# Optimization experiments

Hardware: AMD Instinct MI355X
Metric: run time of the kernel (lower is better)

## Reference

```python
import jax, jax.numpy as jnp
import numpy as np

D_MODEL = 1024
NUM_HEADS = 16
D_K = D_MODEL // NUM_HEADS


def setup_inputs() -> dict:
    key = jax.random.key(0)
    ks = jax.random.split(key, 5)
    B, S = 4, 2048
    scale = 1.0 / np.sqrt(D_MODEL)
    x = jax.random.normal(ks[0], (B, S, D_MODEL), dtype=jnp.float32)
    Wq = jax.random.normal(ks[1], (D_MODEL, D_MODEL), dtype=jnp.float32) * scale
    Wk = jax.random.normal(ks[2], (D_MODEL, D_MODEL), dtype=jnp.float32) * scale
    Wv = jax.random.normal(ks[3], (D_MODEL, D_MODEL), dtype=jnp.float32) * scale
    Wo = jax.random.normal(ks[4], (D_MODEL, D_MODEL), dtype=jnp.float32) * scale
    return {"x": x, "Wq": Wq, "Wk": Wk, "Wv": Wv, "Wo": Wo}


def reference(x, Wq, Wk, Wv, Wo):
    B, S, _ = x.shape
    # projections (torch Linear: y = x @ W^T, no bias)
    def proj(W):
        y = jnp.einsum('bsd,ed->bse', x, W)
        # split heads: (b, s, h*dk) -> (b, h, s, dk)
        return y.reshape(B, S, NUM_HEADS, D_K).transpose(0, 2, 1, 3)
    Q, K, V = proj(Wq), proj(Wk), proj(Wv)
    scores = jnp.einsum('bhqd,bhkd->bhqk', Q, K) / np.sqrt(D_K)
    causal = jnp.tril(jnp.ones((S, S), dtype=bool))
    scores = jnp.where(causal, scores, -jnp.inf)
    attn = jax.nn.softmax(scores, axis=-1)
    out = jnp.einsum('bhqk,bhkd->bhqd', attn, V)
    out = out.transpose(0, 2, 1, 3).reshape(B, S, D_MODEL)
    return jnp.einsum('bse,de->bsd', out, Wo)
```

## Files before the change

### kernel.cpp

```cpp
#include <hip/hip_runtime.h>
#include <hip/hip_bf16.h>

typedef __attribute__((ext_vector_type(8))) short short8;
typedef __attribute__((ext_vector_type(2))) float f32x2;
typedef __attribute__((ext_vector_type(4))) float f32x4;
typedef __attribute__((ext_vector_type(16))) float f32x16;

static constexpr int DM = 1024;
static constexpr int NH = 16;
static constexpr int DK = 64;
static constexpr int SL = 2048;
static constexpr int BB = 4;
static constexpr size_t QKV_ELEMS = (size_t)BB * NH * SL * DK;
static constexpr float NEG_BIG = -30000.0f;
static constexpr float SC_LOG2E = 0.125f * 1.44269504088896340736f;

union PackB { __hip_bfloat16 h[8]; uint4 u; };
union Pack4 { __hip_bfloat16 h[4]; uint2 u; };

typedef __attribute__((address_space(1))) unsigned int gu32;
typedef __attribute__((address_space(3))) unsigned int lu32;
__device__ __forceinline__ void async_copy16(const void* g, void* l) {
    __builtin_amdgcn_global_load_lds((gu32*)g, (lu32*)l, 16, 0, 0);
}

__device__ __forceinline__ unsigned cvt_pk_bf16(float lo, float hi) {
    unsigned r;
    asm("v_cvt_pk_bf16_f32 %0, %1, %2" : "=v"(r) : "v"(lo), "v"(hi));
    return r;
}
__device__ __forceinline__ void pl32_swap(unsigned &a, unsigned &b) {
    asm("v_permlane32_swap_b32 %0, %1" : "+v"(a), "+v"(b));
}

__global__ __launch_bounds__(256)
void cvt_all(const float* __restrict__ x,
             const float* __restrict__ wq, const float* __restrict__ wk,
             const float* __restrict__ wv, const float* __restrict__ wo,
             __hip_bfloat16* __restrict__ dst)
{
    const size_t i = (size_t)blockIdx.x * 256 + threadIdx.x;
    const float* src; size_t local;
    if (i < 2097152) { src = x; local = i; }
    else {
        const size_t j = i - 2097152;
        const int r = (int)(j >> 18);
        local = j & 262143;
        src = (r == 0) ? wq : (r == 1) ? wk : (r == 2) ? wv : wo;
    }
    float4 f = reinterpret_cast<const float4*>(src)[local];
    Pack4 p;
    p.h[0] = __float2bfloat16(f.x); p.h[1] = __float2bfloat16(f.y);
    p.h[2] = __float2bfloat16(f.z); p.h[3] = __float2bfloat16(f.w);
    reinterpret_cast<uint2*>(dst)[i] = p.u;
}

__global__ __launch_bounds__(256)
void gemm_qkv(const __hip_bfloat16* __restrict__ A,
              const __hip_bfloat16* __restrict__ W,
              __hip_bfloat16* __restrict__ q_out,
              __hip_bfloat16* __restrict__ k_out,
              __hip_bfloat16* __restrict__ v_out)
{
    __shared__ __hip_bfloat16 As[2][128 * 64];
    __shared__ __hip_bfloat16 Bs[2][128 * 64];
    const int tid  = threadIdx.x;
    const int m0   = blockIdx.x * 128;
    const int n0   = blockIdx.y * 128;
    const int w    = tid >> 6;
    const int lane = tid & 63;
    const int quad = lane >> 4;
    const int ln   = lane & 15;
    const int wm   = (w & 1) * 64;
    const int wn   = (w >> 1) * 64;
    const int srow = lane >> 3;
    const int sch  = ((lane & 7) ^ srow) * 8;

    f32x4 acc[4][4] = {};

    auto stage = [&](int buf, int k0) {
        #pragma unroll
        for (int j = 0; j < 4; j++) {
            const int rbase = w * 32 + j * 8;
            async_copy16(A + (size_t)(m0 + rbase + srow) * DM + k0 + sch,
                         &As[buf][rbase * 64]);
            async_copy16(W + (size_t)(n0 + rbase + srow) * DM + k0 + sch,
                         &Bs[buf][rbase * 64]);
        }
    };

    constexpr int NT = DM / 64;
    stage(0, 0);
    asm volatile("s_waitcnt vmcnt(0)" ::: "memory");
    __syncthreads();

    int cur = 0;
    for (int t = 0; t < NT; ++t) {
        if (t + 1 < NT) stage(cur ^ 1, (t + 1) * 64);

        #pragma unroll
        for (int ks = 0; ks < 2; ks++) {
            short8 a[4], b[4];
            #pragma unroll
            for (int i = 0; i < 4; i++)
                a[i] = *reinterpret_cast<const short8*>(
                    &As[cur][(wm + i*16 + ln) * 64 + (((ks*4 + quad) ^ (ln & 7)) * 8)]);
            #pragma unroll
            for (int j = 0; j < 4; j++)
                b[j] = *reinterpret_cast<const short8*>(
                    &Bs[cur][(wn + j*16 + ln) * 64 + (((ks*4 + quad) ^ (ln & 7)) * 8)]);
            __builtin_amdgcn_s_setprio(1);
            #pragma unroll
            for (int i = 0; i < 4; i++)
                #pragma unroll
                for (int j = 0; j < 4; j++)
                    acc[i][j] = __builtin_amdgcn_mfma_f32_16x16x32_bf16(a[i], b[j], acc[i][j], 0, 0, 0);
            __builtin_amdgcn_s_setprio(0);
        }

        if (t + 1 < NT) {
            asm volatile("s_waitcnt vmcnt(0)" ::: "memory");
            __syncthreads();
        }
        cur ^= 1;
    }

    #pragma unroll
    for (int i = 0; i < 4; i++) {
        #pragma unroll
        for (int j = 0; j < 4; j++) {
            #pragma unroll
            for (int r = 0; r < 4; r++) {
                const int m = m0 + wm + i*16 + quad*4 + r;
                const int n = n0 + wn + j*16 + ln;
                const int b_ = m >> 11;
                const int s  = m & 2047;
                const int which = n >> 10;
                const int nn = n & 1023;
                const int h  = nn >> 6;
                const int d  = nn & 63;
                if (which == 0) {
                    const __hip_bfloat16 v = __float2bfloat16(acc[i][j][r] * SC_LOG2E);
                    q_out[((size_t)((b_*NH + h)*SL + s))*DK + d] = v;
                } else if (which == 1) {
                    const __hip_bfloat16 v = __float2bfloat16(acc[i][j][r]);
                    k_out[((size_t)((b_*NH + h)*SL + s))*DK + d] = v;
                } else {
                    const __hip_bfloat16 v = __float2bfloat16(acc[i][j][r]);
                    v_out[((size_t)((b_*NH + h)*DK + d))*SL + s] = v;
                }
            }
        }
    }
}

__global__ __launch_bounds__(256)
void gemm_wo(const __hip_bfloat16* __restrict__ A,
             const __hip_bfloat16* __restrict__ W,
             float* __restrict__ outp)
{
    __shared__ __hip_bfloat16 As[2][128 * 64];
    __shared__ __hip_bfloat16 Bs[2][128 * 64];
    const int tid  = threadIdx.x;
    const int m0   = blockIdx.x * 128;
    const int n0   = blockIdx.y * 128;
    const int w    = tid >> 6;
    const int lane = tid & 63;
    const int quad = lane >> 4;
    const int ln   = lane & 15;
    const int wm   = (w & 1) * 64;
    const int wn   = (w >> 1) * 64;
    const int srow = lane >> 3;
    const int sch  = ((lane & 7) ^ srow) * 8;

    f32x4 acc[4][4] = {};

    auto stage = [&](int buf, int k0) {
        #pragma unroll
        for (int j = 0; j < 4; j++) {
            const int rbase = w * 32 + j * 8;
            async_copy16(A + (size_t)(m0 + rbase + srow) * DM + k0 + sch,
                         &As[buf][rbase * 64]);
            async_copy16(W + (size_t)(n0 + rbase + srow) * DM + k0 + sch,
                         &Bs[buf][rbase * 64]);
        }
    };

    constexpr int NT = DM / 64;
    stage(0, 0);
    asm volatile("s_waitcnt vmcnt(0)" ::: "memory");
    __syncthreads();

    int cur = 0;
    for (int t = 0; t < NT; ++t) {
        if (t + 1 < NT) stage(cur ^ 1, (t + 1) * 64);

        #pragma unroll
        for (int ks = 0; ks < 2; ks++) {
            short8 a[4], b[4];
            #pragma unroll
            for (int i = 0; i < 4; i++)
                a[i] = *reinterpret_cast<const short8*>(
                    &As[cur][(wm + i*16 + ln) * 64 + (((ks*4 + quad) ^ (ln & 7)) * 8)]);
            #pragma unroll
            for (int j = 0; j < 4; j++)
                b[j] = *reinterpret_cast<const short8*>(
                    &Bs[cur][(wn + j*16 + ln) * 64 + (((ks*4 + quad) ^ (ln & 7)) * 8)]);
            __builtin_amdgcn_s_setprio(1);
            #pragma unroll
            for (int i = 0; i < 4; i++)
                #pragma unroll
                for (int j = 0; j < 4; j++)
                    acc[i][j] = __builtin_amdgcn_mfma_f32_16x16x32_bf16(a[i], b[j], acc[i][j], 0, 0, 0);
            __builtin_amdgcn_s_setprio(0);
        }

        if (t + 1 < NT) {
            asm volatile("s_waitcnt vmcnt(0)" ::: "memory");
            __syncthreads();
        }
        cur ^= 1;
    }

    #pragma unroll
    for (int i = 0; i < 4; i++)
        #pragma unroll
        for (int j = 0; j < 4; j++)
            #pragma unroll
            for (int r = 0; r < 4; r++) {
                const int m = m0 + wm + i*16 + quad*4 + r;
                const int n = n0 + wn + j*16 + ln;
                outp[(size_t)m * DM + n] = acc[i][j][r];
            }
}

template<bool A_BF16, int MODE>
__global__ __launch_bounds__(256)
void gemm_bt(const void* __restrict__ Ap,
             const float* __restrict__ W,
             void* __restrict__ outp, float scl)
{
    __shared__ __hip_bfloat16 As[128][40];
    __shared__ __hip_bfloat16 Bs[128][40];
    const int tid  = threadIdx.x;
    const int m0   = blockIdx.x * 128;
    const int n0   = blockIdx.y * 128;
    const int w    = tid >> 6;
    const int lane = tid & 63;
    const int quad = lane >> 4;
    const int ln   = lane & 15;
    const int wm   = (w & 1) * 64;
    const int wn   = (w >> 1) * 64;
    const int lr   = tid >> 1;
    const int lc   = (tid & 1) * 16;

    f32x4 acc[4][4] = {};

    for (int k0 = 0; k0 < DM; k0 += 32) {
        if (A_BF16) {
            const uint4* ap = reinterpret_cast<const uint4*>(
                (const __hip_bfloat16*)Ap + (size_t)(m0 + lr) * DM + k0 + lc);
            uint4 a0 = ap[0], a1 = ap[1];
            *reinterpret_cast<uint4*>(&As[lr][lc])     = a0;
            *reinterpret_cast<uint4*>(&As[lr][lc + 8]) = a1;
        } else {
            const float4* ap = reinterpret_cast<const float4*>(
                (const float*)Ap + (size_t)(m0 + lr) * DM + k0 + lc);
            float4 f0 = ap[0], f1 = ap[1], f2 = ap[2], f3 = ap[3];
            PackB p0, p1;
            p0.h[0] = __float2bfloat16(f0.x); p0.h[1] = __float2bfloat16(f0.y);
            p0.h[2] = __float2bfloat16(f0.z); p0.h[3] = __float2bfloat16(f0.w);
            p0.h[4] = __float2bfloat16(f1.x); p0.h[5] = __float2bfloat16(f1.y);
            p0.h[6] = __float2bfloat16(f1.z); p0.h[7] = __float2bfloat16(f1.w);
            p1.h[0] = __float2bfloat16(f2.x); p1.h[1] = __float2bfloat16(f2.y);
            p1.h[2] = __float2bfloat16(f2.z); p1.h[3] = __float2bfloat16(f2.w);
            p1.h[4] = __float2bfloat16(f3.x); p1.h[5] = __float2bfloat16(f3.y);
            p1.h[6] = __float2bfloat16(f3.z); p1.h[7] = __float2bfloat16(f3.w);
            *reinterpret_cast<uint4*>(&As[lr][lc])     = p0.u;
            *reinterpret_cast<uint4*>(&As[lr][lc + 8]) = p1.u;
        }
        {
            const float4* wp = reinterpret_cast<const float4*>(
                W + (size_t)(n0 + lr) * DM + k0 + lc);
            float4 f0 = wp[0], f1 = wp[1], f2 = wp[2], f3 = wp[3];
            PackB p0, p1;
            p0.h[0] = __float2bfloat16(f0.x); p0.h[1] = __float2bfloat16(f0.y);
            p0.h[2] = __float2bfloat16(f0.z); p0.h[3] = __float2bfloat16(f0.w);
            p0.h[4] = __float2bfloat16(f1.x); p0.h[5] = __float2bfloat16(f1.y);
            p0.h[6] = __float2bfloat16(f1.z); p0.h[7] = __float2bfloat16(f1.w);
            p1.h[0] = __float2bfloat16(f2.x); p1.h[1] = __float2bfloat16(f2.y);
            p1.h[2] = __float2bfloat16(f2.z); p1.h[3] = __float2bfloat16(f2.w);
            p1.h[4] = __float2bfloat16(f3.x); p1.h[5] = __float2bfloat16(f3.y);
            p1.h[6] = __float2bfloat16(f3.z); p1.h[7] = __float2bfloat16(f3.w);
            *reinterpret_cast<uint4*>(&Bs[lr][lc])     = p0.u;
            *reinterpret_cast<uint4*>(&Bs[lr][lc + 8]) = p1.u;
        }
        __syncthreads();

        short8 a[4], b[4];
        #pragma unroll
        for (int i = 0; i < 4; i++)
            a[i] = *reinterpret_cast<const short8*>(&As[wm + i*16 + ln][quad*8]);
        #pragma unroll
        for (int j = 0; j < 4; j++)
            b[j] = *reinterpret_cast<const short8*>(&Bs[wn + j*16 + ln][quad*8]);
        #pragma unroll
        for (int i = 0; i < 4; i++)
            #pragma unroll
            for (int j = 0; j < 4; j++)
                acc[i][j] = __builtin_amdgcn_mfma_f32_16x16x32_bf16(a[i], b[j], acc[i][j], 0, 0, 0);
        __syncthreads();
    }

    #pragma unroll
    for (int i = 0; i < 4; i++) {
        #pragma unroll
        for (int j = 0; j < 4; j++) {
            #pragma unroll
            for (int r = 0; r < 4; r++) {
                const int m = m0 + wm + i*16 + quad*4 + r;
                const int n = n0 + wn + j*16 + ln;
                const float v = acc[i][j][r] * scl;
                if (MODE == 2) {
                    ((float*)outp)[(size_t)m * DM + n] = v;
                } else {
                    const int b_ = m >> 11;
                    const int s  = m & 2047;
                    const int h  = n >> 6;
                    const int d  = n & 63;
                    size_t idx;
                    if (MODE == 0) idx = ((size_t)((b_*NH + h)*SL + s))*DK + d;
                    else           idx = ((size_t)((b_*NH + h)*DK + d))*SL + s;
                    ((__hip_bfloat16*)outp)[idx] = __float2bfloat16(v);
                }
            }
        }
    }
}

__global__ __launch_bounds__(256)
void attn_causal(const __hip_bfloat16* __restrict__ Q,
                 const __hip_bfloat16* __restrict__ K,
                 const __hip_bfloat16* __restrict__ Vt,
                 __hip_bfloat16* __restrict__ O)
{
    __shared__ __hip_bfloat16 Ks[128 * 64];
    __shared__ __hip_bfloat16 Vs[64 * 128];

    const int tid  = threadIdx.x;
    const int w    = tid >> 6;
    const int lane = tid & 63;
    const int ln32 = lane & 31;
    const int hi   = lane >> 5;
    const int bh   = blockIdx.y;
    const int b_   = bh >> 4;
    const int h    = bh & 15;

    const __hip_bfloat16* Qb = Q  + (size_t)bh * SL * DK;
    const __hip_bfloat16* Kb = K  + (size_t)bh * SL * DK;
    const __hip_bfloat16* Vb = Vt + (size_t)bh * DK * SL;

    for (int pass = 0; pass < 2; ++pass) {
        const int qt    = (pass == 0) ? (int)blockIdx.x : 15 - (int)blockIdx.x;
        const int q0    = qt * 128;
        const int qbase = q0 + w * 32;
        const int qg    = qbase + ln32;

        short8 qf[4];
        #pragma unroll
        for (int dt = 0; dt < 4; dt++)
            qf[dt] = *reinterpret_cast<const short8*>(
                Qb + (size_t)qg * DK + dt*16 + hi*8);

        f32x16 o0 = {}, o1 = {};
        f32x2 ls2 = {0.f, 0.f};

        const int npair = qt + 1;

        for (int ip = 0; ip < npair; ++ip) {
            const int k0 = ip * 128;
            #pragma unroll
            for (int j = 0; j < 4; j++) {
                const int rb = w * 32 + j * 8;
                const int r  = rb + (lane >> 3);
                async_copy16(Kb + (size_t)(k0 + r) * DK + (((lane & 7) ^ (r & 7)) * 8),
                             &Ks[rb * 64]);
            }
            #pragma unroll
            for (int j = 0; j < 4; j++) {
                const int db = w * 16 + j * 4;
                const int d  = db + (lane >> 4);
                async_copy16(Vb + (size_t)d * SL + k0 + (((lane & 15) ^ (d & 7)) * 8),
                             &Vs[db * 128]);
            }
            asm volatile("s_waitcnt vmcnt(0)" ::: "memory");
            __syncthreads();

            #pragma unroll
            for (int hf = 0; hf < 2; hf++) {
                const int kh0 = k0 + hf * 64;
                if (kh0 > qbase + 31) continue;

                f32x16 s0 = {}, s1 = {};
                __builtin_amdgcn_s_setprio(1);
                #pragma unroll
                for (int dt = 0; dt < 4; dt++) {
                    const int r0 = hf*64 + ln32;
                    const int ch = (dt*2 + hi) ^ (ln32 & 7);
                    short8 kf0 = *reinterpret_cast<const short8*>(&Ks[r0*64 + ch*8]);
                    short8 kf1 = *reinterpret_cast<const short8*>(&Ks[(r0 + 32)*64 + ch*8]);
                    s0 = __builtin_amdgcn_mfma_f32_32x32x16_bf16(kf0, qf[dt], s0, 0, 0, 0);
                    s1 = __builtin_amdgcn_mfma_f32_32x32x16_bf16(kf1, qf[dt], s1, 0, 0, 0);
                }
                __builtin_amdgcn_s_setprio(0);

                const bool dodiag = (kh0 + 63 > qbase);
                if (dodiag) {
                    #pragma unroll
                    for (int r = 0; r < 16; r++) {
                        const int km = (r & 3) + 8*(r >> 2) + 4*hi;
                        float v0 = s0[r];
                        float v1 = s1[r];
                        if (kh0 + km      > qg) v0 = NEG_BIG;
                        if (kh0 + 32 + km > qg) v1 = NEG_BIG;
                        const float p0 = __builtin_amdgcn_exp2f(v0);
                        const float p1 = __builtin_amdgcn_exp2f(v1);
                        s0[r] = p0; s1[r] = p1;
                        ls2.x += p0; ls2.y += p1;
                    }
                } else {
                    #pragma unroll
                    for (int r = 0; r < 16; r++) {
                        const float p0 = __builtin_amdgcn_exp2f(s0[r]);
                        const float p1 = __builtin_amdgcn_exp2f(s1[r]);
                        s0[r] = p0; s1[r] = p1;
                        ls2.x += p0; ls2.y += p1;
                    }
                }

                __builtin_amdgcn_s_setprio(1);
                #pragma unroll
                for (int c = 0; c < 4; c++) {
                    const int R = 8 * (c & 1);
                    unsigned x0, x1, y0, y1;
                    if (c < 2) {
                        x0 = cvt_pk_bf16(s0[R+0], s0[R+1]);
                        x1 = cvt_pk_bf16(s0[R+2], s0[R+3]);
                        y0 = cvt_pk_bf16(s0[R+4], s0[R+5]);
                        y1 = cvt_pk_bf16(s0[R+6], s0[R+7]);
                    } else {
                        x0 = cvt_pk_bf16(s1[R+0], s1[R+1]);
                        x1 = cvt_pk_bf16(s1[R+2], s1[R+3]);
                        y0 = cvt_pk_bf16(s1[R+4], s1[R+5]);
                        y1 = cvt_pk_bf16(s1[R+6], s1[R+7]);
                    }
                    pl32_swap(x0, y0);
                    pl32_swap(x1, y1);
                    union { unsigned u[4]; short8 s8; } pf;
                    pf.u[0] = x0; pf.u[1] = x1; pf.u[2] = y0; pf.u[3] = y1;
                    const int vc = (hf*8 + c*2 + hi) ^ (ln32 & 7);
                    short8 vf0 = *reinterpret_cast<const short8*>(&Vs[ln32*128 + vc*8]);
                    short8 vf1 = *reinterpret_cast<const short8*>(&Vs[(32 + ln32)*128 + vc*8]);
                    o0 = __builtin_amdgcn_mfma_f32_32x32x16_bf16(vf0, pf.s8, o0, 0, 0, 0);
                    o1 = __builtin_amdgcn_mfma_f32_32x32x16_bf16(vf1, pf.s8, o1, 0, 0, 0);
                }
                __builtin_amdgcn_s_setprio(0);
            }
            __syncthreads();
        }

        float lsum = ls2.x + ls2.y;
        const float ls = lsum + __shfl_xor(lsum, 32, 64);
        const float rq = 1.0f / ls;

        __hip_bfloat16* Orow = O + (((size_t)b_ * SL + qg) * NH + h) * DK;
        #pragma unroll
        for (int g = 0; g < 4; g++) {
            uint2 pk0, pk1;
            pk0.x = cvt_pk_bf16(o0[4*g+0]*rq, o0[4*g+1]*rq);
            pk0.y = cvt_pk_bf16(o0[4*g+2]*rq, o0[4*g+3]*rq);
            pk1.x = cvt_pk_bf16(o1[4*g+0]*rq, o1[4*g+1]*rq);
            pk1.y = cvt_pk_bf16(o1[4*g+2]*rq, o1[4*g+3]*rq);
            *reinterpret_cast<uint2*>(Orow + 8*g + 4*hi)      = pk0;
            *reinterpret_cast<uint2*>(Orow + 32 + 8*g + 4*hi) = pk1;
        }
    }
}

extern "C" void kernel_launch(void* const* d_in, const int* in_sizes, int n_in,
                              void* d_out, int out_size, void* d_ws, size_t ws_size,
                              hipStream_t stream)
{
    const float* x  = (const float*)d_in[0];
    const float* Wq = (const float*)d_in[1];
    const float* Wk = (const float*)d_in[2];
    const float* Wv = (const float*)d_in[3];
    const float* Wo = (const float*)d_in[4];

    __hip_bfloat16* q_ws = (__hip_bfloat16*)d_ws;
    __hip_bfloat16* k_ws = q_ws + QKV_ELEMS;
    __hip_bfloat16* v_ws = k_ws + QKV_ELEMS;

    const dim3 gb(256);
    const size_t FAST_WS = (3 * QKV_ELEMS + QKV_ELEMS + 4 * (size_t)DM * DM)
                           * sizeof(__hip_bfloat16);

    if (ws_size >= FAST_WS) {
        __hip_bfloat16* xb  = v_ws + QKV_ELEMS;
        __hip_bfloat16* wqb = xb  + QKV_ELEMS;
        __hip_bfloat16* wob = wqb + 3 * (size_t)DM * DM;

        cvt_all<<<12288, 256, 0, stream>>>(x, Wq, Wk, Wv, Wo, xb);

        gemm_qkv<<<dim3(64, 24), gb, 0, stream>>>(xb, wqb, q_ws, k_ws, v_ws);

        attn_causal<<<dim3(8, BB*NH), 256, 0, stream>>>(q_ws, k_ws, v_ws, xb);

        gemm_wo<<<dim3(64, 8), gb, 0, stream>>>(xb, wob, (float*)d_out);
    } else {
        __hip_bfloat16* obuf = (__hip_bfloat16*)d_out;
        float*          fbuf = (float*)d_ws;
        const dim3 gg(64, 8);
        gemm_bt<false, 0><<<gg, gb, 0, stream>>>(x, Wq, q_ws, SC_LOG2E);
        gemm_bt<false, 0><<<gg, gb, 0, stream>>>(x, Wk, k_ws, 1.0f);
        gemm_bt<false, 1><<<gg, gb, 0, stream>>>(x, Wv, v_ws, 1.0f);
        attn_causal<<<dim3(8, BB*NH), 256, 0, stream>>>(q_ws, k_ws, v_ws, obuf);
        gemm_bt<true, 2><<<gg, gb, 0, stream>>>(obuf, Wo, fbuf, 1.0f);
        (void)hipMemcpyAsync(d_out, fbuf, QKV_ELEMS * sizeof(float),
                             hipMemcpyDeviceToDevice, stream);
    }
}
```

Baseline: 249.9 us.

## Use 256x128 GEMM tiles with 512 threads and a triple-buffered async pipeline

Both bf16 projection GEMMs (QKV and output) now use 512-thread blocks that compute 256x128 output tiles, with eight waves arranged 4x2. Shared memory becomes a three-stage ring, so loads run two K-tiles ahead. Each wait uses vmcnt(6) to wait only for the older stage, and sched_barriers surround the raw s_barrier. The aim is more reuse of each staged W tile and better hiding of global-to-LDS latency. The cost is about 144KB of LDS per block, which allows only one block per CU, and fewer blocks in the grid, which may leave the GPU with a coarser tail.

```diff
diff --git a/kernel.cpp b/kernel.cpp
--- a/kernel.cpp
+++ b/kernel.cpp
@@ -55,24 +55,24 @@
     reinterpret_cast<uint2*>(dst)[i] = p.u;
 }
 
-__global__ __launch_bounds__(256)
+__global__ __launch_bounds__(512, 2)
 void gemm_qkv(const __hip_bfloat16* __restrict__ A,
               const __hip_bfloat16* __restrict__ W,
               __hip_bfloat16* __restrict__ q_out,
               __hip_bfloat16* __restrict__ k_out,
               __hip_bfloat16* __restrict__ v_out)
 {
-    __shared__ __hip_bfloat16 As[2][128 * 64];
-    __shared__ __hip_bfloat16 Bs[2][128 * 64];
+    __shared__ __hip_bfloat16 As[3][256 * 64];
+    __shared__ __hip_bfloat16 Bs[3][128 * 64];
     const int tid  = threadIdx.x;
-    const int m0   = blockIdx.x * 128;
+    const int m0   = blockIdx.x * 256;
     const int n0   = blockIdx.y * 128;
     const int w    = tid >> 6;
     const int lane = tid & 63;
     const int quad = lane >> 4;
     const int ln   = lane & 15;
-    const int wm   = (w & 1) * 64;
-    const int wn   = (w >> 1) * 64;
+    const int wm   = (w & 3) * 64;
+    const int wn   = (w >> 2) * 64;
     const int srow = lane >> 3;
     const int sch  = ((lane & 7) ^ srow) * 8;
 
@@ -84,6 +84,10 @@
             const int rbase = w * 32 + j * 8;
             async_copy16(A + (size_t)(m0 + rbase + srow) * DM + k0 + sch,
                          &As[buf][rbase * 64]);
+        }
+        #pragma unroll
+        for (int j = 0; j < 2; j++) {
+            const int rbase = w * 16 + j * 8;
             async_copy16(W + (size_t)(n0 + rbase + srow) * DM + k0 + sch,
                          &Bs[buf][rbase * 64]);
         }
@@ -91,12 +95,15 @@
 
     constexpr int NT = DM / 64;
     stage(0, 0);
-    asm volatile("s_waitcnt vmcnt(0)" ::: "memory");
-    __syncthreads();
-
-    int cur = 0;
+    stage(1, 64);
+    asm volatile("s_waitcnt vmcnt(6)" ::: "memory");
+    __builtin_amdgcn_sched_barrier(0);
+    __builtin_amdgcn_s_barrier();
+    __builtin_amdgcn_sched_barrier(0);
+
     for (int t = 0; t < NT; ++t) {
-        if (t + 1 < NT) stage(cur ^ 1, (t + 1) * 64);
+        const int cur = t % 3;
+        if (t + 2 < NT) stage((t + 2) % 3, (t + 2) * 64);
 
         #pragma unroll
         for (int ks = 0; ks < 2; ks++) {
@@ -118,11 +125,17 @@
             __builtin_amdgcn_s_setprio(0);
         }
 
-        if (t + 1 < NT) {
+        if (t + 2 < NT) {
+            asm volatile("s_waitcnt vmcnt(6)" ::: "memory");
+            __builtin_amdgcn_sched_barrier(0);
+            __builtin_amdgcn_s_barrier();
+            __builtin_amdgcn_sched_barrier(0);
+        } else if (t + 1 < NT) {
             asm volatile("s_waitcnt vmcnt(0)" ::: "memory");
-            __syncthreads();
-        }
-        cur ^= 1;
+            __builtin_amdgcn_sched_barrier(0);
+            __builtin_amdgcn_s_barrier();
+            __builtin_amdgcn_sched_barrier(0);
+        }
     }
 
     #pragma unroll
@@ -154,22 +167,22 @@
     }
 }
 
-__global__ __launch_bounds__(256)
+__global__ __launch_bounds__(512, 2)
 void gemm_wo(const __hip_bfloat16* __restrict__ A,
              const __hip_bfloat16* __restrict__ W,
              float* __restrict__ outp)
 {
-    __shared__ __hip_bfloat16 As[2][128 * 64];
-    __shared__ __hip_bfloat16 Bs[2][128 * 64];
+    __shared__ __hip_bfloat16 As[3][256 * 64];
+    __shared__ __hip_bfloat16 Bs[3][128 * 64];
     const int tid  = threadIdx.x;
-    const int m0   = blockIdx.x * 128;
+    const int m0   = blockIdx.x * 256;
     const int n0   = blockIdx.y * 128;
     const int w    = tid >> 6;
     const int lane = tid & 63;
     const int quad = lane >> 4;
     const int ln   = lane & 15;
-    const int wm   = (w & 1) * 64;
-    const int wn   = (w >> 1) * 64;
+    const int wm   = (w & 3) * 64;
+    const int wn   = (w >> 2) * 64;
     const int srow = lane >> 3;
     const int sch  = ((lane & 7) ^ srow) * 8;
 
@@ -181,6 +194,10 @@
             const int rbase = w * 32 + j * 8;
             async_copy16(A + (size_t)(m0 + rbase + srow) * DM + k0 + sch,
                          &As[buf][rbase * 64]);
+        }
+        #pragma unroll
+        for (int j = 0; j < 2; j++) {
+            const int rbase = w * 16 + j * 8;
             async_copy16(W + (size_t)(n0 + rbase + srow) * DM + k0 + sch,
                          &Bs[buf][rbase * 64]);
         }
@@ -188,12 +205,15 @@
 
     constexpr int NT = DM / 64;
     stage(0, 0);
-    asm volatile("s_waitcnt vmcnt(0)" ::: "memory");
-    __syncthreads();
-
-    int cur = 0;
+    stage(1, 64);
+    asm volatile("s_waitcnt vmcnt(6)" ::: "memory");
+    __builtin_amdgcn_sched_barrier(0);
+    __builtin_amdgcn_s_barrier();
+    __builtin_amdgcn_sched_barrier(0);
+
     for (int t = 0; t < NT; ++t) {
-        if (t + 1 < NT) stage(cur ^ 1, (t + 1) * 64);
+        const int cur = t % 3;
+        if (t + 2 < NT) stage((t + 2) % 3, (t + 2) * 64);
 
         #pragma unroll
         for (int ks = 0; ks < 2; ks++) {
@@ -215,11 +235,17 @@
             __builtin_amdgcn_s_setprio(0);
         }
 
-        if (t + 1 < NT) {
+        if (t + 2 < NT) {
+            asm volatile("s_waitcnt vmcnt(6)" ::: "memory");
+            __builtin_amdgcn_sched_barrier(0);
+            __builtin_amdgcn_s_barrier();
+            __builtin_amdgcn_sched_barrier(0);
+        } else if (t + 1 < NT) {
             asm volatile("s_waitcnt vmcnt(0)" ::: "memory");
-            __syncthreads();
-        }
-        cur ^= 1;
+            __builtin_amdgcn_sched_barrier(0);
+            __builtin_amdgcn_s_barrier();
+            __builtin_amdgcn_sched_barrier(0);
+        }
     }
 
     #pragma unroll
@@ -501,7 +527,6 @@
     __hip_bfloat16* k_ws = q_ws + QKV_ELEMS;
     __hip_bfloat16* v_ws = k_ws + QKV_ELEMS;
 
-    const dim3 gb(256);
     const size_t FAST_WS = (3 * QKV_ELEMS + QKV_ELEMS + 4 * (size_t)DM * DM)
                            * sizeof(__hip_bfloat16);
 
@@ -512,15 +537,16 @@
 
         cvt_all<<<12288, 256, 0, stream>>>(x, Wq, Wk, Wv, Wo, xb);
 
-        gemm_qkv<<<dim3(64, 24), gb, 0, stream>>>(xb, wqb, q_ws, k_ws, v_ws);
+        gemm_qkv<<<dim3(32, 24), dim3(512), 0, stream>>>(xb, wqb, q_ws, k_ws, v_ws);
 
         attn_causal<<<dim3(8, BB*NH), 256, 0, stream>>>(q_ws, k_ws, v_ws, xb);
 
-        gemm_wo<<<dim3(64, 8), gb, 0, stream>>>(xb, wob, (float*)d_out);
+        gemm_wo<<<dim3(32, 8), dim3(512), 0, stream>>>(xb, wob, (float*)d_out);
     } else {
         __hip_bfloat16* obuf = (__hip_bfloat16*)d_out;
         float*          fbuf = (float*)d_ws;
         const dim3 gg(64, 8);
+        const dim3 gb(256);
         gemm_bt<false, 0><<<gg, gb, 0, stream>>>(x, Wq, q_ws, SC_LOG2E);
         gemm_bt<false, 0><<<gg, gb, 0, stream>>>(x, Wk, k_ws, 1.0f);
         gemm_bt<false, 1><<<gg, gb, 0, stream>>>(x, Wv, v_ws, 1.0f);
```

New measurement: 264.9 us. 1.06x slower.

## Double-buffer K/V tiles in causal attention to overlap loads with MFMA

Applied to the files above, without the earlier changes.

The attention kernel now keeps two LDS buffers for K and V and issues the async global-to-LDS copy for the next 128-key tile before computing on the current one. It waits with vmcnt(8) so only the current tile's copies must land. The goal is to hide global load latency behind the QK and PV matrix work. In exchange LDS use per block doubles to 64KB, which may lower occupancy, and correctness now depends on the barrier and vmcnt bookkeeping.

```diff
diff --git a/kernel.cpp b/kernel.cpp
--- a/kernel.cpp
+++ b/kernel.cpp
@@ -344,8 +344,8 @@
                  const __hip_bfloat16* __restrict__ Vt,
                  __hip_bfloat16* __restrict__ O)
 {
-    __shared__ __hip_bfloat16 Ks[128 * 64];
-    __shared__ __hip_bfloat16 Vs[64 * 128];
+    __shared__ __hip_bfloat16 Ks[2][128 * 64];
+    __shared__ __hip_bfloat16 Vs[2][64 * 128];
 
     const int tid  = threadIdx.x;
     const int w    = tid >> 6;
@@ -360,6 +360,23 @@
     const __hip_bfloat16* Kb = K  + (size_t)bh * SL * DK;
     const __hip_bfloat16* Vb = Vt + (size_t)bh * DK * SL;
 
+    auto stageKV = [&](int buf, int k0) {
+        #pragma unroll
+        for (int j = 0; j < 4; j++) {
+            const int rb = w * 32 + j * 8;
+            const int r  = rb + (lane >> 3);
+            async_copy16(Kb + (size_t)(k0 + r) * DK + (((lane & 7) ^ (r & 7)) * 8),
+                         &Ks[buf][rb * 64]);
+        }
+        #pragma unroll
+        for (int j = 0; j < 4; j++) {
+            const int db = w * 16 + j * 4;
+            const int d  = db + (lane >> 4);
+            async_copy16(Vb + (size_t)d * SL + k0 + (((lane & 15) ^ (d & 7)) * 8),
+                         &Vs[buf][db * 128]);
+        }
+    };
+
     for (int pass = 0; pass < 2; ++pass) {
         const int qt    = (pass == 0) ? (int)blockIdx.x : 15 - (int)blockIdx.x;
         const int q0    = qt * 128;
@@ -377,25 +394,21 @@
 
         const int npair = qt + 1;
 
+        stageKV(0, 0);
+
         for (int ip = 0; ip < npair; ++ip) {
+            const int cur = ip & 1;
+            if (ip + 1 < npair) {
+                stageKV(cur ^ 1, (ip + 1) * 128);
+                asm volatile("s_waitcnt vmcnt(8)" ::: "memory");
+            } else {
+                asm volatile("s_waitcnt vmcnt(0)" ::: "memory");
+            }
+            __builtin_amdgcn_sched_barrier(0);
+            __builtin_amdgcn_s_barrier();
+            __builtin_amdgcn_sched_barrier(0);
+
             const int k0 = ip * 128;
-            #pragma unroll
-            for (int j = 0; j < 4; j++) {
-                const int rb = w * 32 + j * 8;
-                const int r  = rb + (lane >> 3);
-                async_copy16(Kb + (size_t)(k0 + r) * DK + (((lane & 7) ^ (r & 7)) * 8),
-                             &Ks[rb * 64]);
-            }
-            #pragma unroll
-            for (int j = 0; j < 4; j++) {
-                const int db = w * 16 + j * 4;
-                const int d  = db + (lane >> 4);
-                async_copy16(Vb + (size_t)d * SL + k0 + (((lane & 15) ^ (d & 7)) * 8),
-                             &Vs[db * 128]);
-            }
-            asm volatile("s_waitcnt vmcnt(0)" ::: "memory");
-            __syncthreads();
-
             #pragma unroll
             for (int hf = 0; hf < 2; hf++) {
                 const int kh0 = k0 + hf * 64;
@@ -407,8 +420,8 @@
                 for (int dt = 0; dt < 4; dt++) {
                     const int r0 = hf*64 + ln32;
                     const int ch = (dt*2 + hi) ^ (ln32 & 7);
-                    short8 kf0 = *reinterpret_cast<const short8*>(&Ks[r0*64 + ch*8]);
-                    short8 kf1 = *reinterpret_cast<const short8*>(&Ks[(r0 + 32)*64 + ch*8]);
+                    short8 kf0 = *reinterpret_cast<const short8*>(&Ks[cur][r0*64 + ch*8]);
+                    short8 kf1 = *reinterpret_cast<const short8*>(&Ks[cur][(r0 + 32)*64 + ch*8]);
                     s0 = __builtin_amdgcn_mfma_f32_32x32x16_bf16(kf0, qf[dt], s0, 0, 0, 0);
                     s1 = __builtin_amdgcn_mfma_f32_32x32x16_bf16(kf1, qf[dt], s1, 0, 0, 0);
                 }
@@ -459,14 +472,14 @@
                     union { unsigned u[4]; short8 s8; } pf;
                     pf.u[0] = x0; pf.u[1] = x1; pf.u[2] = y0; pf.u[3] = y1;
                     const int vc = (hf*8 + c*2 + hi) ^ (ln32 & 7);
-                    short8 vf0 = *reinterpret_cast<const short8*>(&Vs[ln32*128 + vc*8]);
-                    short8 vf1 = *reinterpret_cast<const short8*>(&Vs[(32 + ln32)*128 + vc*8]);
+                    short8 vf0 = *reinterpret_cast<const short8*>(&Vs[cur][ln32*128 + vc*8]);
+                    short8 vf1 = *reinterpret_cast<const short8*>(&Vs[cur][(32 + ln32)*128 + vc*8]);
                     o0 = __builtin_amdgcn_mfma_f32_32x32x16_bf16(vf0, pf.s8, o0, 0, 0, 0);
                     o1 = __builtin_amdgcn_mfma_f32_32x32x16_bf16(vf1, pf.s8, o1, 0, 0, 0);
                 }
                 __builtin_amdgcn_s_setprio(0);
             }
-            __syncthreads();
+            __builtin_amdgcn_s_barrier();
         }
 
         float lsum = ls2.x + ls2.y;
```

Measured after the change: 248.1 us. About the same (-0.7%).
